# Kernel optimization log

Measured on AMD Instinct MI355X. Metric: run time of the kernel, lower is better.

## Reference

```python
import jax, jax.numpy as jnp
import numpy as np

D_MODEL = 1024
H = 16
D_K = D_MODEL // H
B = 2
S = 2048
NEG = -1e10


def setup_inputs() -> dict:
    key = jax.random.key(0)
    ks = jax.random.split(key, 12)
    sc = 1.0 / np.sqrt(D_MODEL)
    inp = {
        "q": jax.random.normal(ks[0], (B, S, D_MODEL), jnp.float32),
        "k": jax.random.normal(ks[1], (B, S, D_MODEL), jnp.float32),
        "v": jax.random.normal(ks[2], (B, S, D_MODEL), jnp.float32),
        # causal mask, broadcast over batch and heads
        "mask": jnp.tril(jnp.ones((S, S), jnp.int32))[None, None, :, :],
        "w_q": jax.random.normal(ks[3], (D_MODEL, D_MODEL), jnp.float32) * sc,
        "b_q": jax.random.normal(ks[4], (D_MODEL,), jnp.float32) * sc,
        "w_k": jax.random.normal(ks[5], (D_MODEL, D_MODEL), jnp.float32) * sc,
        "b_k": jax.random.normal(ks[6], (D_MODEL,), jnp.float32) * sc,
        "w_v": jax.random.normal(ks[7], (D_MODEL, D_MODEL), jnp.float32) * sc,
        "b_v": jax.random.normal(ks[8], (D_MODEL,), jnp.float32) * sc,
        "w_o": jax.random.normal(ks[9], (D_MODEL, D_MODEL), jnp.float32) * sc,
        "b_o": jax.random.normal(ks[10], (D_MODEL,), jnp.float32) * sc,
    }
    return inp


def _split_heads(x):
    # [B, S, D] -> [B, H, S, d_k]
    b, s, _ = x.shape
    return x.reshape(b, s, H, D_K).transpose(0, 2, 1, 3)


def reference(q, k, v, mask, w_q, b_q, w_k, b_k, w_v, b_v, w_o, b_o):
    # Linear projections (torch Linear: x @ W.T + b)
    qh = _split_heads(q @ w_q.T + b_q)
    kh = _split_heads(k @ w_k.T + b_k)
    vh = _split_heads(v @ w_v.T + b_v)
    scale = 1.0 / jnp.sqrt(jnp.asarray(D_K, qh.dtype))
    scores = jnp.einsum("bhqd,bhkd->bhqk", qh, kh) * scale
    scores = jnp.where(mask == 0, jnp.asarray(NEG, scores.dtype), scores)
    attn = jax.nn.softmax(scores, axis=-1)  # dropout=0.0 -> identity
    x = jnp.einsum("bhqk,bhkd->bhqd", attn, vh)
    x = x.transpose(0, 2, 1, 3).reshape(q.shape[0], -1, H * D_K)
    out = x @ w_o.T + b_o
    return (out, attn)
```

## Files before the change

kernel.cpp:

```cpp
#include <hip/hip_runtime.h>
#include <hip/hip_bf16.h>

typedef unsigned short u16;
typedef unsigned int u32;
typedef __attribute__((ext_vector_type(8))) short bf16x8;
typedef __attribute__((ext_vector_type(4))) float f32x4;

#define SEQ 2048
#define DM 1024
#define NH 16
#define DKK 64
#define NB 2

__device__ __forceinline__ u16 f2bf(float f) {
  union { float f; u32 u; } x; x.f = f;
  u32 r = x.u + 0x7FFFu + ((x.u >> 16) & 1u);
  return (u16)(r >> 16);
}

__device__ __forceinline__ void gl_lds16(const void* g, void* l) {
  __builtin_amdgcn_global_load_lds(
      (const __attribute__((address_space(1))) u32*)g,
      (__attribute__((address_space(3))) u32*)l, 16, 0, 0);
}

__device__ __forceinline__ void nt_store4(float* p, f32x4 v) {
  __builtin_nontemporal_store(v, (f32x4*)p);
}

#define MFMA16(a, b, c) __builtin_amdgcn_mfma_f32_16x16x32_bf16(a, b, c, 0, 0, 0)
#define VMCNT0() asm volatile("s_waitcnt vmcnt(0)" ::: "memory")
#define VMCNT4() asm volatile("s_waitcnt vmcnt(4)" ::: "memory")
#define SCHEDB() __builtin_amdgcn_sched_barrier(0)

struct CvtArgs {
  const float* in[7];
  u16* out[7];
  int n4[7];
};

__global__ __launch_bounds__(256) void cvt_all(CvtArgs a) {
  const int y = blockIdx.y;
  const float* in = a.in[y];
  u16* out = a.out[y];
  const int n4 = a.n4[y];
  int i = blockIdx.x * 256 + threadIdx.x;
  if (i >= n4) return;
  float4 v = ((const float4*)in)[i];
  ushort4 o;
  o.x = f2bf(v.x); o.y = f2bf(v.y); o.z = f2bf(v.z); o.w = f2bf(v.w);
  ((ushort4*)out)[i] = o;
}

struct ProjArgs {
  const u16* A;
  const u16* W;
  const float* bias;
  u16* Y;
  float scale;
};

__global__ __launch_bounds__(256) void proj_qkv(ProjArgs a0, ProjArgs a1,
                                                ProjArgs a2) {
  ProjArgs pa = (blockIdx.z == 0) ? a0 : (blockIdx.z == 1) ? a1 : a2;
  __shared__ __align__(16) u16 As[2][128 * 32];
  __shared__ __align__(16) u16 Bs[2][128 * 32];
  const int tid = threadIdx.x, lane = tid & 63, w = tid >> 6;
  const int lr = lane & 15, lg = lane >> 4;
  const int wr = w >> 1, wc = w & 1;
  const int c0 = blockIdx.x * 128, r0 = blockIdx.y * 128;
  f32x4 acc[4][4];
#pragma unroll
  for (int i = 0; i < 4; ++i)
#pragma unroll
    for (int j = 0; j < 4; ++j) acc[i][j] = (f32x4){0.f, 0.f, 0.f, 0.f};

  auto stage = [&](int k0, int buf) {
#pragma unroll
    for (int c = 0; c < 2; ++c) {
      int idx = tid + 256 * c;
      int row = idx >> 2, seg = idx & 3;
      gl_lds16(pa.A + (size_t)(r0 + row) * DM + k0 + seg * 8,
               (char*)As[buf] + idx * 16);
      gl_lds16(pa.W + (size_t)(c0 + row) * DM + k0 + seg * 8,
               (char*)Bs[buf] + idx * 16);
    }
  };

  stage(0, 0);
  __syncthreads();
  int buf = 0;
  const int NT = DM / 32;
  for (int t = 0; t < NT; ++t) {
    if (t + 1 < NT) stage((t + 1) * 32, buf ^ 1);
    bf16x8 a[4], b[4];
#pragma unroll
    for (int i = 0; i < 4; ++i) {
      int row = wr * 64 + i * 16 + lr;
      a[i] = *(const bf16x8*)((const char*)As[buf] + row * 64 + lg * 16);
    }
#pragma unroll
    for (int j = 0; j < 4; ++j) {
      int row = wc * 64 + j * 16 + lr;
      b[j] = *(const bf16x8*)((const char*)Bs[buf] + row * 64 + lg * 16);
    }
#pragma unroll
    for (int i = 0; i < 4; ++i)
#pragma unroll
      for (int j = 0; j < 4; ++j) acc[i][j] = MFMA16(a[i], b[j], acc[i][j]);
    __syncthreads();
    buf ^= 1;
  }
#pragma unroll
  for (int i = 0; i < 4; ++i)
#pragma unroll
    for (int j = 0; j < 4; ++j)
#pragma unroll
      for (int rg = 0; rg < 4; ++rg) {
        int row = r0 + wr * 64 + i * 16 + lg * 4 + rg;
        int col = c0 + wc * 64 + j * 16 + lr;
        float v = (acc[i][j][rg] + pa.bias[col]) * pa.scale;
        int bb = row >> 11, s = row & (SEQ - 1), h = col >> 6, d = col & 63;
        pa.Y[((size_t)(bb * NH + h) * SEQ + s) * DKK + d] = f2bf(v);
      }
}

__global__ __launch_bounds__(256) void mm_out(const u16* __restrict__ A,
                                              const u16* __restrict__ W,
                                              const float* __restrict__ bias,
                                              float* __restrict__ Y) {
  __shared__ __align__(16) u16 As[2][128 * 32];
  __shared__ __align__(16) u16 Bs[2][128 * 32];
  const int tid = threadIdx.x, lane = tid & 63, w = tid >> 6;
  const int lr = lane & 15, lg = lane >> 4;
  const int wr = w >> 1, wc = w & 1;
  const int c0 = blockIdx.x * 128, r0 = blockIdx.y * 128;
  f32x4 acc[4][4];
#pragma unroll
  for (int i = 0; i < 4; ++i)
#pragma unroll
    for (int j = 0; j < 4; ++j) acc[i][j] = (f32x4){0.f, 0.f, 0.f, 0.f};

  auto stage = [&](int k0, int buf) {
#pragma unroll
    for (int c = 0; c < 2; ++c) {
      int idx = tid + 256 * c;
      int row = idx >> 2, seg = idx & 3;
      gl_lds16(A + (size_t)(r0 + row) * DM + k0 + seg * 8,
               (char*)As[buf] + idx * 16);
      gl_lds16(W + (size_t)(c0 + row) * DM + k0 + seg * 8,
               (char*)Bs[buf] + idx * 16);
    }
  };

  stage(0, 0);
  __syncthreads();
  int buf = 0;
  const int NT = DM / 32;
  for (int t = 0; t < NT; ++t) {
    if (t + 1 < NT) stage((t + 1) * 32, buf ^ 1);
    bf16x8 a[4], b[4];
#pragma unroll
    for (int i = 0; i < 4; ++i) {
      int row = wr * 64 + i * 16 + lr;
      a[i] = *(const bf16x8*)((const char*)As[buf] + row * 64 + lg * 16);
    }
#pragma unroll
    for (int j = 0; j < 4; ++j) {
      int row = wc * 64 + j * 16 + lr;
      b[j] = *(const bf16x8*)((const char*)Bs[buf] + row * 64 + lg * 16);
    }
#pragma unroll
    for (int i = 0; i < 4; ++i)
#pragma unroll
      for (int j = 0; j < 4; ++j) acc[i][j] = MFMA16(a[i], b[j], acc[i][j]);
    __syncthreads();
    buf ^= 1;
  }
#pragma unroll
  for (int i = 0; i < 4; ++i)
#pragma unroll
    for (int j = 0; j < 4; ++j)
#pragma unroll
      for (int rg = 0; rg < 4; ++rg) {
        int row = r0 + wr * 64 + i * 16 + lg * 4 + rg;
        int col = c0 + wc * 64 + j * 16 + lr;
        Y[(size_t)row * DM + col] = acc[i][j][rg] + bias[col];
      }
}

__global__ __launch_bounds__(256) void transpose_v(const u16* __restrict__ Vh,
                                                   u16* __restrict__ Vt) {
  const int st = blockIdx.x, bh = blockIdx.y;
  const u16* src = Vh + ((size_t)bh * SEQ + st * 64) * DKK;
  u16* dst = Vt + (size_t)bh * DKK * SEQ + st * 64;
  __shared__ u16 T[64][68];
  const int tid = threadIdx.x;
#pragma unroll
  for (int c = 0; c < 4; ++c) {
    int idx = tid + 256 * c;
    int r = idx >> 4, seg = idx & 15;
    ushort4 v = *(const ushort4*)(src + r * 64 + seg * 4);
    *(ushort4*)&T[r][seg * 4] = v;
  }
  __syncthreads();
#pragma unroll
  for (int c = 0; c < 4; ++c) {
    int idx = tid + 256 * c;
    int d = idx >> 4, sseg = idx & 15;
    ushort4 o;
    o.x = T[sseg * 4 + 0][d]; o.y = T[sseg * 4 + 1][d];
    o.z = T[sseg * 4 + 2][d]; o.w = T[sseg * 4 + 3][d];
    *(ushort4*)(dst + (size_t)d * SEQ + sseg * 4) = o;
  }
}

__global__ __launch_bounds__(256) void flash_attn(const u16* __restrict__ Qh,
                                                  const u16* __restrict__ Kh,
                                                  const u16* __restrict__ Vt,
                                                  u16* __restrict__ X,
                                                  float* __restrict__ attn) {
  const int lin = (int)(blockIdx.y * gridDim.x + blockIdx.x);
  const int swz = (lin & 7) * 128 + (lin >> 3);
  const int qi = 31 - (swz & 31);
  const int bh = swz >> 5;
  const int q0 = qi * 64;
  const u16* Qb = Qh + (size_t)bh * SEQ * DKK;
  const u16* Kb = Kh + (size_t)bh * SEQ * DKK;
  const u16* Vb = Vt + (size_t)bh * DKK * SEQ;
  float* attb = attn + (size_t)bh * SEQ * SEQ;
  const int tid = threadIdx.x, lane = tid & 63, w = tid >> 6;
  const int lr = lane & 15, lg = lane >> 4;

  __shared__ __align__(16) u16 Ks[2][64 * 64];
  __shared__ __align__(16) u16 Vs[2][64 * 64];
  __shared__ __align__(16) u16 Ps[4 * 16 * 64];

  bf16x8 frQ[2];
#pragma unroll
  for (int kc = 0; kc < 2; ++kc) {
    int r = q0 + w * 16 + lr;
    frQ[kc] = *(const bf16x8*)(Qb + (size_t)r * DKK + kc * 32 + lg * 8);
  }

  const int qglob = q0 + w * 16 + lr;
  const int wmax = q0 + w * 16 + 15;
  const int nkv = qi + 1;

  auto stageK = [&](int j, int buf) {
    const int kv0 = j * 64;
#pragma unroll
    for (int c = 0; c < 2; ++c) {
      int idx = tid + 256 * c;
      int row = idx >> 3, sq = idx & 7;
      int seg = sq ^ (row & 7);
      gl_lds16(Kb + (size_t)(kv0 + row) * DKK + seg * 8,
               (char*)Ks[buf] + idx * 16);
    }
  };
  auto stageV = [&](int j, int buf) {
    const int kv0 = j * 64;
#pragma unroll
    for (int c = 0; c < 2; ++c) {
      int idx = tid + 256 * c;
      int row = idx >> 3, sq = idx & 7;
      int seg = sq ^ (row & 7);
      gl_lds16(Vb + (size_t)row * SEQ + kv0 + seg * 8,
               (char*)Vs[buf] + idx * 16);
    }
  };

  float rs = 0.f;
  stageK(0, 0);
  VMCNT0();
  __builtin_amdgcn_s_barrier();
  SCHEDB();
  for (int j = 0; j < nkv; ++j) {
    const int buf = j & 1;
    const int kv0 = j * 64;
    if (j + 1 < nkv) stageK(j + 1, buf ^ 1);
    if (kv0 <= wmax) {
      __builtin_amdgcn_s_setprio(1);
#pragma unroll
      for (int ci = 0; ci < 4; ++ci) {
        bf16x8 aK[2];
#pragma unroll
        for (int kc = 0; kc < 2; ++kc) {
          int row = ci * 16 + lr;
          int q = (kc * 4 + lg) ^ (row & 7);
          aK[kc] = *(const bf16x8*)((const char*)Ks[buf] + row * 128 + q * 16);
        }
        f32x4 a = (f32x4){0.f, 0.f, 0.f, 0.f};
        a = MFMA16(aK[0], frQ[0], a);
        a = MFMA16(aK[1], frQ[1], a);
#pragma unroll
        for (int rg = 0; rg < 4; ++rg) {
          int kvglob = kv0 + ci * 16 + lg * 4 + rg;
          rs += (kvglob <= qglob) ? __expf(a[rg]) : 0.f;
        }
      }
      __builtin_amdgcn_s_setprio(0);
    }
    VMCNT0();
    __builtin_amdgcn_s_barrier();
    SCHEDB();
  }
  rs += __shfl_xor(rs, 16);
  rs += __shfl_xor(rs, 32);
  const float vinv = 1.f / rs;

  f32x4 accO[4];
#pragma unroll
  for (int ci = 0; ci < 4; ++ci) accO[ci] = (f32x4){0.f, 0.f, 0.f, 0.f};

  stageK(0, 0);
  stageV(0, 0);
  VMCNT0();
  __builtin_amdgcn_s_barrier();
  SCHEDB();
  for (int j = 0; j < nkv; ++j) {
    const int buf = j & 1;
    const int kv0 = j * 64;
    if (j + 1 < nkv) {
      stageK(j + 1, buf ^ 1);
      stageV(j + 1, buf ^ 1);
    }
    if (kv0 <= wmax) {
      __builtin_amdgcn_s_setprio(1);
      f32x4 sf[4];
#pragma unroll
      for (int ci = 0; ci < 4; ++ci) {
        bf16x8 aK[2];
#pragma unroll
        for (int kc = 0; kc < 2; ++kc) {
          int row = ci * 16 + lr;
          int q = (kc * 4 + lg) ^ (row & 7);
          aK[kc] = *(const bf16x8*)((const char*)Ks[buf] + row * 128 + q * 16);
        }
        f32x4 a = (f32x4){0.f, 0.f, 0.f, 0.f};
        a = MFMA16(aK[0], frQ[0], a);
        a = MFMA16(aK[1], frQ[1], a);
        sf[ci] = a;
      }
      float* orow = attb + (size_t)qglob * SEQ;
#pragma unroll
      for (int ci = 0; ci < 4; ++ci) {
        float p[4];
#pragma unroll
        for (int rg = 0; rg < 4; ++rg) {
          int kvglob = kv0 + ci * 16 + lg * 4 + rg;
          p[rg] = (kvglob <= qglob) ? __expf(sf[ci][rg]) * vinv : 0.f;
        }
        f32x4 o = {p[0], p[1], p[2], p[3]};
        nt_store4(orow + kv0 + ci * 16 + lg * 4, o);
        u32 lo = (u32)f2bf(p[0]) | ((u32)f2bf(p[1]) << 16);
        u32 hi = (u32)f2bf(p[2]) | ((u32)f2bf(p[3]) << 16);
        int c16 = (ci * 2 + (lg >> 1)) ^ (lr & 7);
        char* dst = (char*)Ps + w * 2048 + lr * 128 + c16 * 16 + (lg & 1) * 8;
        *(uint2*)dst = (uint2){lo, hi};
      }
#pragma unroll
      for (int kvc = 0; kvc < 2; ++kvc) {
        int c16a = (kvc * 4 + lg) ^ (lr & 7);
        bf16x8 aP =
            *(const bf16x8*)((const char*)Ps + w * 2048 + lr * 128 + c16a * 16);
#pragma unroll
        for (int ci = 0; ci < 4; ++ci) {
          int row = ci * 16 + lr;
          int q2 = (kvc * 4 + lg) ^ (row & 7);
          bf16x8 bV =
              *(const bf16x8*)((const char*)Vs[buf] + row * 128 + q2 * 16);
          accO[ci] = MFMA16(aP, bV, accO[ci]);
        }
      }
      __builtin_amdgcn_s_setprio(0);
    } else {
      const f32x4 z = {0.f, 0.f, 0.f, 0.f};
      float* orow = attb + (size_t)qglob * SEQ;
#pragma unroll
      for (int ci = 0; ci < 4; ++ci)
        nt_store4(orow + kv0 + ci * 16 + lg * 4, z);
    }
    VMCNT4();
    __builtin_amdgcn_s_barrier();
    SCHEDB();
  }

  {
    const f32x4 z = {0.f, 0.f, 0.f, 0.f};
    float* orow = attb + (size_t)qglob * SEQ;
    for (int j = nkv; j < SEQ / 64; ++j) {
      const int kv0 = j * 64;
#pragma unroll
      for (int ci = 0; ci < 4; ++ci)
        nt_store4(orow + kv0 + ci * 16 + lg * 4, z);
    }
  }

  const int b = bh >> 4, h = bh & (NH - 1);
#pragma unroll
  for (int ci = 0; ci < 4; ++ci)
#pragma unroll
    for (int rg = 0; rg < 4; ++rg) {
      int srow = q0 + w * 16 + lg * 4 + rg;
      int col = h * DKK + ci * 16 + lr;
      X[((size_t)(b * SEQ + srow)) * DM + col] = f2bf(accO[ci][rg]);
    }
}

extern "C" void kernel_launch(void* const* d_in, const int* in_sizes, int n_in,
                              void* d_out, int out_size, void* d_ws,
                              size_t ws_size, hipStream_t stream) {
  const float* q = (const float*)d_in[0];
  const float* k = (const float*)d_in[1];
  const float* v = (const float*)d_in[2];
  const float* w_q = (const float*)d_in[4];
  const float* b_q = (const float*)d_in[5];
  const float* w_k = (const float*)d_in[6];
  const float* b_k = (const float*)d_in[7];
  const float* w_v = (const float*)d_in[8];
  const float* b_v = (const float*)d_in[9];
  const float* w_o = (const float*)d_in[10];
  const float* b_o = (const float*)d_in[11];

  float* out = (float*)d_out;
  float* attn = out + (size_t)NB * SEQ * DM;

  const size_t MB = 1u << 20;
  char* ws = (char*)d_ws;
  u16* qb = (u16*)(ws);
  u16* kb = (u16*)(ws + 8 * MB);
  u16* vb = (u16*)(ws + 16 * MB);
  u16* Qh = (u16*)(ws + 24 * MB);
  u16* Kh = (u16*)(ws + 32 * MB);
  u16* Vh = (u16*)(ws + 40 * MB);
  u16* wqb = (u16*)(ws + 48 * MB);
  u16* wkb = (u16*)(ws + 50 * MB);
  u16* wvb = (u16*)(ws + 52 * MB);
  u16* wob = (u16*)(ws + 54 * MB);
  u16* Vt = qb;
  u16* X = vb;

  dim3 blk(256);
  const int n4_qkv = NB * SEQ * DM / 4;
  const int n4_w = DM * DM / 4;

  CvtArgs ca;
  ca.in[0] = q;   ca.out[0] = qb;  ca.n4[0] = n4_qkv;
  ca.in[1] = k;   ca.out[1] = kb;  ca.n4[1] = n4_qkv;
  ca.in[2] = v;   ca.out[2] = vb;  ca.n4[2] = n4_qkv;
  ca.in[3] = w_q; ca.out[3] = wqb; ca.n4[3] = n4_w;
  ca.in[4] = w_k; ca.out[4] = wkb; ca.n4[4] = n4_w;
  ca.in[5] = w_v; ca.out[5] = wvb; ca.n4[5] = n4_w;
  ca.in[6] = w_o; ca.out[6] = wob; ca.n4[6] = n4_w;
  cvt_all<<<dim3((n4_qkv + 255) / 256, 7), blk, 0, stream>>>(ca);

  ProjArgs aq = {qb, wqb, b_q, Qh, 0.125f};
  ProjArgs ak = {kb, wkb, b_k, Kh, 1.0f};
  ProjArgs av = {vb, wvb, b_v, Vh, 1.0f};
  proj_qkv<<<dim3(DM / 128, NB * SEQ / 128, 3), blk, 0, stream>>>(aq, ak, av);

  transpose_v<<<dim3(SEQ / 64, NB * NH), blk, 0, stream>>>(Vh, Vt);

  flash_attn<<<dim3(SEQ / 64, NB * NH), blk, 0, stream>>>(Qh, Kh, Vt, X, attn);

  mm_out<<<dim3(DM / 128, NB * SEQ / 128), blk, 0, stream>>>(X, wob, b_o, out);
}
```

Baseline: 325.9 us.

## Fuse all stages into one persistent megakernel with grid-wide atomic barriers

After: 736.6 us. 126% more time.

```diff
diff --git a/kernel.cpp b/kernel.cpp
--- a/kernel.cpp
+++ b/kernel.cpp
@@ -11,6 +11,7 @@
 #define NH 16
 #define DKK 64
 #define NB 2
+#define NBLK 512
 
 __device__ __forceinline__ u16 f2bf(float f) {
   union { float f; u32 u; } x; x.f = f;
@@ -24,120 +25,47 @@
       (__attribute__((address_space(3))) u32*)l, 16, 0, 0);
 }
 
-__device__ __forceinline__ void nt_store4(float* p, f32x4 v) {
-  __builtin_nontemporal_store(v, (f32x4*)p);
-}
-
 #define MFMA16(a, b, c) __builtin_amdgcn_mfma_f32_16x16x32_bf16(a, b, c, 0, 0, 0)
 #define VMCNT0() asm volatile("s_waitcnt vmcnt(0)" ::: "memory")
-#define VMCNT4() asm volatile("s_waitcnt vmcnt(4)" ::: "memory")
 #define SCHEDB() __builtin_amdgcn_sched_barrier(0)
 
-struct CvtArgs {
-  const float* in[7];
-  u16* out[7];
-  int n4[7];
+__device__ __forceinline__ void gbar(int* cnt, int idx) {
+  __syncthreads();
+  if (threadIdx.x == 0) {
+    __threadfence();
+    __hip_atomic_fetch_add(&cnt[idx], 1, __ATOMIC_RELEASE,
+                           __HIP_MEMORY_SCOPE_AGENT);
+    while (__hip_atomic_load(&cnt[idx], __ATOMIC_ACQUIRE,
+                             __HIP_MEMORY_SCOPE_AGENT) < NBLK) {
+      __builtin_amdgcn_s_sleep(8);
+    }
+    __threadfence();
+  }
+  __syncthreads();
+}
+
+struct MegaArgs {
+  const float *q, *k, *v;
+  const float *wq, *bq, *wk, *bk, *wv, *bv, *wo, *bo;
+  u16 *qb, *kb, *vb;
+  u16 *Qh, *Kh, *Vh;
+  u16 *wqb, *wkb, *wvb, *wob;
+  u16 *Vt, *X;
+  float *out, *attn;
+  int *cnt;
 };
 
-__global__ __launch_bounds__(256) void cvt_all(CvtArgs a) {
-  const int y = blockIdx.y;
-  const float* in = a.in[y];
-  u16* out = a.out[y];
-  const int n4 = a.n4[y];
-  int i = blockIdx.x * 256 + threadIdx.x;
-  if (i >= n4) return;
-  float4 v = ((const float4*)in)[i];
-  ushort4 o;
-  o.x = f2bf(v.x); o.y = f2bf(v.y); o.z = f2bf(v.z); o.w = f2bf(v.w);
-  ((ushort4*)out)[i] = o;
-}
-
-struct ProjArgs {
-  const u16* A;
-  const u16* W;
-  const float* bias;
-  u16* Y;
-  float scale;
-};
-
-__global__ __launch_bounds__(256) void proj_qkv(ProjArgs a0, ProjArgs a1,
-                                                ProjArgs a2) {
-  ProjArgs pa = (blockIdx.z == 0) ? a0 : (blockIdx.z == 1) ? a1 : a2;
-  __shared__ __align__(16) u16 As[2][128 * 32];
-  __shared__ __align__(16) u16 Bs[2][128 * 32];
-  const int tid = threadIdx.x, lane = tid & 63, w = tid >> 6;
+template <int MODE>
+__device__ void gemm128x64(const u16* __restrict__ A, const u16* __restrict__ Wm,
+                           const float* __restrict__ bias, u16* Yh, float* Yf,
+                           float scale, int r0, int c0, char* LDSp, int tid) {
+  char* As = LDSp;
+  char* Bs = LDSp + 16384;
+  const int lane = tid & 63, w = tid >> 6;
   const int lr = lane & 15, lg = lane >> 4;
-  const int wr = w >> 1, wc = w & 1;
-  const int c0 = blockIdx.x * 128, r0 = blockIdx.y * 128;
-  f32x4 acc[4][4];
-#pragma unroll
-  for (int i = 0; i < 4; ++i)
-#pragma unroll
-    for (int j = 0; j < 4; ++j) acc[i][j] = (f32x4){0.f, 0.f, 0.f, 0.f};
-
-  auto stage = [&](int k0, int buf) {
-#pragma unroll
-    for (int c = 0; c < 2; ++c) {
-      int idx = tid + 256 * c;
-      int row = idx >> 2, seg = idx & 3;
-      gl_lds16(pa.A + (size_t)(r0 + row) * DM + k0 + seg * 8,
-               (char*)As[buf] + idx * 16);
-      gl_lds16(pa.W + (size_t)(c0 + row) * DM + k0 + seg * 8,
-               (char*)Bs[buf] + idx * 16);
-    }
-  };
-
-  stage(0, 0);
-  __syncthreads();
-  int buf = 0;
-  const int NT = DM / 32;
-  for (int t = 0; t < NT; ++t) {
-    if (t + 1 < NT) stage((t + 1) * 32, buf ^ 1);
-    bf16x8 a[4], b[4];
-#pragma unroll
-    for (int i = 0; i < 4; ++i) {
-      int row = wr * 64 + i * 16 + lr;
-      a[i] = *(const bf16x8*)((const char*)As[buf] + row * 64 + lg * 16);
-    }
-#pragma unroll
-    for (int j = 0; j < 4; ++j) {
-      int row = wc * 64 + j * 16 + lr;
-      b[j] = *(const bf16x8*)((const char*)Bs[buf] + row * 64 + lg * 16);
-    }
-#pragma unroll
-    for (int i = 0; i < 4; ++i)
-#pragma unroll
-      for (int j = 0; j < 4; ++j) acc[i][j] = MFMA16(a[i], b[j], acc[i][j]);
-    __syncthreads();
-    buf ^= 1;
-  }
-#pragma unroll
-  for (int i = 0; i < 4; ++i)
-#pragma unroll
-    for (int j = 0; j < 4; ++j)
-#pragma unroll
-      for (int rg = 0; rg < 4; ++rg) {
-        int row = r0 + wr * 64 + i * 16 + lg * 4 + rg;
-        int col = c0 + wc * 64 + j * 16 + lr;
-        float v = (acc[i][j][rg] + pa.bias[col]) * pa.scale;
-        int bb = row >> 11, s = row & (SEQ - 1), h = col >> 6, d = col & 63;
-        pa.Y[((size_t)(bb * NH + h) * SEQ + s) * DKK + d] = f2bf(v);
-      }
-}
-
-__global__ __launch_bounds__(256) void mm_out(const u16* __restrict__ A,
-                                              const u16* __restrict__ W,
-                                              const float* __restrict__ bias,
-                                              float* __restrict__ Y) {
-  __shared__ __align__(16) u16 As[2][128 * 32];
-  __shared__ __align__(16) u16 Bs[2][128 * 32];
-  const int tid = threadIdx.x, lane = tid & 63, w = tid >> 6;
-  const int lr = lane & 15, lg = lane >> 4;
-  const int wr = w >> 1, wc = w & 1;
-  const int c0 = blockIdx.x * 128, r0 = blockIdx.y * 128;
-  f32x4 acc[4][4];
-#pragma unroll
-  for (int i = 0; i < 4; ++i)
+  f32x4 acc[2][4];
+#pragma unroll
+  for (int i = 0; i < 2; ++i)
 #pragma unroll
     for (int j = 0; j < 4; ++j) acc[i][j] = (f32x4){0.f, 0.f, 0.f, 0.f};
 
@@ -147,105 +75,76 @@
       int idx = tid + 256 * c;
       int row = idx >> 2, seg = idx & 3;
       gl_lds16(A + (size_t)(r0 + row) * DM + k0 + seg * 8,
-               (char*)As[buf] + idx * 16);
-      gl_lds16(W + (size_t)(c0 + row) * DM + k0 + seg * 8,
-               (char*)Bs[buf] + idx * 16);
+               As + buf * 8192 + idx * 16);
+    }
+    {
+      int row = tid >> 2, seg = tid & 3;
+      gl_lds16(Wm + (size_t)(c0 + row) * DM + k0 + seg * 8,
+               Bs + buf * 4096 + tid * 16);
     }
   };
 
   stage(0, 0);
   __syncthreads();
   int buf = 0;
-  const int NT = DM / 32;
-  for (int t = 0; t < NT; ++t) {
-    if (t + 1 < NT) stage((t + 1) * 32, buf ^ 1);
-    bf16x8 a[4], b[4];
-#pragma unroll
-    for (int i = 0; i < 4; ++i) {
-      int row = wr * 64 + i * 16 + lr;
-      a[i] = *(const bf16x8*)((const char*)As[buf] + row * 64 + lg * 16);
+#pragma unroll 1
+  for (int t = 0; t < DM / 32; ++t) {
+    if (t + 1 < DM / 32) stage((t + 1) * 32, buf ^ 1);
+    bf16x8 aa[2], bb[4];
+#pragma unroll
+    for (int i = 0; i < 2; ++i) {
+      int row = w * 32 + i * 16 + lr;
+      aa[i] = *(const bf16x8*)(As + buf * 8192 + row * 64 + lg * 16);
     }
 #pragma unroll
     for (int j = 0; j < 4; ++j) {
-      int row = wc * 64 + j * 16 + lr;
-      b[j] = *(const bf16x8*)((const char*)Bs[buf] + row * 64 + lg * 16);
-    }
-#pragma unroll
-    for (int i = 0; i < 4; ++i)
-#pragma unroll
-      for (int j = 0; j < 4; ++j) acc[i][j] = MFMA16(a[i], b[j], acc[i][j]);
+      int row2 = j * 16 + lr;
+      bb[j] = *(const bf16x8*)(Bs + buf * 4096 + row2 * 64 + lg * 16);
+    }
+#pragma unroll
+    for (int i = 0; i < 2; ++i)
+#pragma unroll
+      for (int j = 0; j < 4; ++j) acc[i][j] = MFMA16(aa[i], bb[j], acc[i][j]);
     __syncthreads();
     buf ^= 1;
   }
 #pragma unroll
-  for (int i = 0; i < 4; ++i)
+  for (int i = 0; i < 2; ++i)
 #pragma unroll
     for (int j = 0; j < 4; ++j)
 #pragma unroll
       for (int rg = 0; rg < 4; ++rg) {
-        int row = r0 + wr * 64 + i * 16 + lg * 4 + rg;
-        int col = c0 + wc * 64 + j * 16 + lr;
-        Y[(size_t)row * DM + col] = acc[i][j][rg] + bias[col];
-      }
-}
-
-__global__ __launch_bounds__(256) void transpose_v(const u16* __restrict__ Vh,
-                                                   u16* __restrict__ Vt) {
-  const int st = blockIdx.x, bh = blockIdx.y;
-  const u16* src = Vh + ((size_t)bh * SEQ + st * 64) * DKK;
-  u16* dst = Vt + (size_t)bh * DKK * SEQ + st * 64;
-  __shared__ u16 T[64][68];
-  const int tid = threadIdx.x;
-#pragma unroll
-  for (int c = 0; c < 4; ++c) {
-    int idx = tid + 256 * c;
-    int r = idx >> 4, seg = idx & 15;
-    ushort4 v = *(const ushort4*)(src + r * 64 + seg * 4);
-    *(ushort4*)&T[r][seg * 4] = v;
-  }
-  __syncthreads();
-#pragma unroll
-  for (int c = 0; c < 4; ++c) {
-    int idx = tid + 256 * c;
-    int d = idx >> 4, sseg = idx & 15;
-    ushort4 o;
-    o.x = T[sseg * 4 + 0][d]; o.y = T[sseg * 4 + 1][d];
-    o.z = T[sseg * 4 + 2][d]; o.w = T[sseg * 4 + 3][d];
-    *(ushort4*)(dst + (size_t)d * SEQ + sseg * 4) = o;
-  }
-}
-
-__global__ __launch_bounds__(256) void flash_attn(const u16* __restrict__ Qh,
-                                                  const u16* __restrict__ Kh,
-                                                  const u16* __restrict__ Vt,
-                                                  u16* __restrict__ X,
-                                                  float* __restrict__ attn) {
-  const int lin = (int)(blockIdx.y * gridDim.x + blockIdx.x);
-  const int swz = (lin & 7) * 128 + (lin >> 3);
-  const int qi = 31 - (swz & 31);
-  const int bh = swz >> 5;
+        int row = r0 + w * 32 + i * 16 + lg * 4 + rg;
+        int col = c0 + j * 16 + lr;
+        if (MODE == 0) {
+          float v = (acc[i][j][rg] + bias[col]) * scale;
+          int bb2 = row >> 11, s = row & (SEQ - 1);
+          int h = col >> 6, d = col & 63;
+          Yh[((size_t)(bb2 * NH + h) * SEQ + s) * DKK + d] = f2bf(v);
+        } else {
+          Yf[(size_t)row * DM + col] = acc[i][j][rg] + bias[col];
+        }
+      }
+}
+
+__device__ void flash64(const u16* __restrict__ Qb, const u16* __restrict__ Kb,
+                        const u16* __restrict__ Vb, u16* __restrict__ X,
+                        float* __restrict__ attb, int bh, int qi, char* LDSp,
+                        int tid) {
+  char* Ks = LDSp;
+  char* Vs = LDSp + 16384;
+  char* Ps = LDSp + 32768;
+  const int lane = tid & 63, w = tid >> 6;
+  const int lr = lane & 15, lg = lane >> 4;
   const int q0 = qi * 64;
-  const u16* Qb = Qh + (size_t)bh * SEQ * DKK;
-  const u16* Kb = Kh + (size_t)bh * SEQ * DKK;
-  const u16* Vb = Vt + (size_t)bh * DKK * SEQ;
-  float* attb = attn + (size_t)bh * SEQ * SEQ;
-  const int tid = threadIdx.x, lane = tid & 63, w = tid >> 6;
-  const int lr = lane & 15, lg = lane >> 4;
-
-  __shared__ __align__(16) u16 Ks[2][64 * 64];
-  __shared__ __align__(16) u16 Vs[2][64 * 64];
-  __shared__ __align__(16) u16 Ps[4 * 16 * 64];
-
-  bf16x8 frQ[2];
-#pragma unroll
-  for (int kc = 0; kc < 2; ++kc) {
-    int r = q0 + w * 16 + lr;
-    frQ[kc] = *(const bf16x8*)(Qb + (size_t)r * DKK + kc * 32 + lg * 8);
-  }
-
   const int qglob = q0 + w * 16 + lr;
   const int wmax = q0 + w * 16 + 15;
   const int nkv = qi + 1;
+
+  bf16x8 frQ[2];
+#pragma unroll
+  for (int kc = 0; kc < 2; ++kc)
+    frQ[kc] = *(const bf16x8*)(Qb + (size_t)qglob * DKK + kc * 32 + lg * 8);
 
   auto stageK = [&](int j, int buf) {
     const int kv0 = j * 64;
@@ -255,7 +154,7 @@
       int row = idx >> 3, sq = idx & 7;
       int seg = sq ^ (row & 7);
       gl_lds16(Kb + (size_t)(kv0 + row) * DKK + seg * 8,
-               (char*)Ks[buf] + idx * 16);
+               Ks + buf * 8192 + idx * 16);
     }
   };
   auto stageV = [&](int j, int buf) {
@@ -266,7 +165,7 @@
       int row = idx >> 3, sq = idx & 7;
       int seg = sq ^ (row & 7);
       gl_lds16(Vb + (size_t)row * SEQ + kv0 + seg * 8,
-               (char*)Vs[buf] + idx * 16);
+               Vs + buf * 8192 + idx * 16);
     }
   };
 
@@ -287,8 +186,8 @@
 #pragma unroll
         for (int kc = 0; kc < 2; ++kc) {
           int row = ci * 16 + lr;
-          int q = (kc * 4 + lg) ^ (row & 7);
-          aK[kc] = *(const bf16x8*)((const char*)Ks[buf] + row * 128 + q * 16);
+          int qq = (kc * 4 + lg) ^ (row & 7);
+          aK[kc] = *(const bf16x8*)(Ks + buf * 8192 + row * 128 + qq * 16);
         }
         f32x4 a = (f32x4){0.f, 0.f, 0.f, 0.f};
         a = MFMA16(aK[0], frQ[0], a);
@@ -325,6 +224,7 @@
       stageK(j + 1, buf ^ 1);
       stageV(j + 1, buf ^ 1);
     }
+    float* orow = attb + (size_t)qglob * SEQ;
     if (kv0 <= wmax) {
       __builtin_amdgcn_s_setprio(1);
       f32x4 sf[4];
@@ -334,15 +234,14 @@
 #pragma unroll
         for (int kc = 0; kc < 2; ++kc) {
           int row = ci * 16 + lr;
-          int q = (kc * 4 + lg) ^ (row & 7);
-          aK[kc] = *(const bf16x8*)((const char*)Ks[buf] + row * 128 + q * 16);
+          int qq = (kc * 4 + lg) ^ (row & 7);
+          aK[kc] = *(const bf16x8*)(Ks + buf * 8192 + row * 128 + qq * 16);
         }
         f32x4 a = (f32x4){0.f, 0.f, 0.f, 0.f};
         a = MFMA16(aK[0], frQ[0], a);
         a = MFMA16(aK[1], frQ[1], a);
         sf[ci] = a;
       }
-      float* orow = attb + (size_t)qglob * SEQ;
 #pragma unroll
       for (int ci = 0; ci < 4; ++ci) {
         float p[4];
@@ -352,36 +251,33 @@
           p[rg] = (kvglob <= qglob) ? __expf(sf[ci][rg]) * vinv : 0.f;
         }
         f32x4 o = {p[0], p[1], p[2], p[3]};
-        nt_store4(orow + kv0 + ci * 16 + lg * 4, o);
+        *(f32x4*)(orow + kv0 + ci * 16 + lg * 4) = o;
         u32 lo = (u32)f2bf(p[0]) | ((u32)f2bf(p[1]) << 16);
         u32 hi = (u32)f2bf(p[2]) | ((u32)f2bf(p[3]) << 16);
         int c16 = (ci * 2 + (lg >> 1)) ^ (lr & 7);
-        char* dst = (char*)Ps + w * 2048 + lr * 128 + c16 * 16 + (lg & 1) * 8;
+        char* dst = Ps + w * 2048 + lr * 128 + c16 * 16 + (lg & 1) * 8;
         *(uint2*)dst = (uint2){lo, hi};
       }
 #pragma unroll
       for (int kvc = 0; kvc < 2; ++kvc) {
         int c16a = (kvc * 4 + lg) ^ (lr & 7);
-        bf16x8 aP =
-            *(const bf16x8*)((const char*)Ps + w * 2048 + lr * 128 + c16a * 16);
+        bf16x8 aP = *(const bf16x8*)(Ps + w * 2048 + lr * 128 + c16a * 16);
 #pragma unroll
         for (int ci = 0; ci < 4; ++ci) {
           int row = ci * 16 + lr;
           int q2 = (kvc * 4 + lg) ^ (row & 7);
-          bf16x8 bV =
-              *(const bf16x8*)((const char*)Vs[buf] + row * 128 + q2 * 16);
+          bf16x8 bV = *(const bf16x8*)(Vs + buf * 8192 + row * 128 + q2 * 16);
           accO[ci] = MFMA16(aP, bV, accO[ci]);
         }
       }
       __builtin_amdgcn_s_setprio(0);
     } else {
       const f32x4 z = {0.f, 0.f, 0.f, 0.f};
-      float* orow = attb + (size_t)qglob * SEQ;
 #pragma unroll
       for (int ci = 0; ci < 4; ++ci)
-        nt_store4(orow + kv0 + ci * 16 + lg * 4, z);
-    }
-    VMCNT4();
+        *(f32x4*)(orow + kv0 + ci * 16 + lg * 4) = z;
+    }
+    VMCNT0();
     __builtin_amdgcn_s_barrier();
     SCHEDB();
   }
@@ -393,7 +289,7 @@
       const int kv0 = j * 64;
 #pragma unroll
       for (int ci = 0; ci < 4; ++ci)
-        nt_store4(orow + kv0 + ci * 16 + lg * 4, z);
+        *(f32x4*)(orow + kv0 + ci * 16 + lg * 4) = z;
     }
   }
 
@@ -408,61 +304,139 @@
     }
 }
 
+__global__ __launch_bounds__(256, 2) void mega(MegaArgs a) {
+  __shared__ __align__(16) char LDS[40 * 1024];
+  const int tid = threadIdx.x, bid = (int)blockIdx.x;
+
+  {
+    const int base = bid * 256 + tid;
+#pragma unroll 4
+    for (int it = 0; it < 32; ++it) {
+      int i = base + it * (NBLK * 256);
+      const float* in;
+      u16* outp;
+      int loc;
+      if (i < 3145728) {
+        int t = i >> 20;
+        loc = i & 1048575;
+        in = (t == 0) ? a.q : (t == 1) ? a.k : a.v;
+        outp = (t == 0) ? a.qb : (t == 1) ? a.kb : a.vb;
+      } else {
+        int j2 = i - 3145728;
+        int t = j2 >> 18;
+        loc = j2 & 262143;
+        in = (t == 0) ? a.wq : (t == 1) ? a.wk : (t == 2) ? a.wv : a.wo;
+        outp = (t == 0) ? a.wqb : (t == 1) ? a.wkb : (t == 2) ? a.wvb : a.wob;
+      }
+      float4 vv = ((const float4*)in)[loc];
+      ushort4 o;
+      o.x = f2bf(vv.x); o.y = f2bf(vv.y); o.z = f2bf(vv.z); o.w = f2bf(vv.w);
+      ((ushort4*)outp)[loc] = o;
+    }
+  }
+  gbar(a.cnt, 0);
+
+  for (int s = 0; s < 3; ++s) {
+    int job = bid + s * NBLK;
+    int g = job >> 9;
+    int jl = job & 511;
+    int ct = jl & 15, rt = jl >> 4;
+    const u16* A = (g == 0) ? a.qb : (g == 1) ? a.kb : a.vb;
+    const u16* Wm = (g == 0) ? a.wqb : (g == 1) ? a.wkb : a.wvb;
+    const float* bias = (g == 0) ? a.bq : (g == 1) ? a.bk : a.bv;
+    u16* Y = (g == 0) ? a.Qh : (g == 1) ? a.Kh : a.Vh;
+    float scale = (g == 0) ? 0.125f : 1.0f;
+    gemm128x64<0>(A, Wm, bias, Y, nullptr, scale, rt * 128, ct * 64, LDS, tid);
+    __syncthreads();
+  }
+  gbar(a.cnt, 1);
+
+  for (int s = 0; s < 2; ++s) {
+    int job = bid + s * NBLK;
+    int st = job & 31, bh = job >> 5;
+    const u16* src = a.Vh + ((size_t)bh * SEQ + st * 64) * DKK;
+    u16* dst = a.Vt + (size_t)bh * DKK * SEQ + st * 64;
+    u16(*T)[68] = (u16(*)[68])LDS;
+#pragma unroll
+    for (int c = 0; c < 4; ++c) {
+      int idx = tid + 256 * c;
+      int r = idx >> 4, seg = idx & 15;
+      ushort4 v = *(const ushort4*)(src + r * 64 + seg * 4);
+      *(ushort4*)&T[r][seg * 4] = v;
+    }
+    __syncthreads();
+#pragma unroll
+    for (int c = 0; c < 4; ++c) {
+      int idx = tid + 256 * c;
+      int d = idx >> 4, sseg = idx & 15;
+      ushort4 o;
+      o.x = T[sseg * 4 + 0][d]; o.y = T[sseg * 4 + 1][d];
+      o.z = T[sseg * 4 + 2][d]; o.w = T[sseg * 4 + 3][d];
+      *(ushort4*)(dst + (size_t)d * SEQ + sseg * 4) = o;
+    }
+    __syncthreads();
+  }
+  gbar(a.cnt, 2);
+
+  {
+    const int iq = bid & 15, bh = bid >> 4;
+    const u16* Qb = a.Qh + (size_t)bh * SEQ * DKK;
+    const u16* Kb = a.Kh + (size_t)bh * SEQ * DKK;
+    const u16* Vb = a.Vt + (size_t)bh * DKK * SEQ;
+    float* attb = a.attn + (size_t)bh * SEQ * SEQ;
+#pragma unroll 1
+    for (int pp = 0; pp < 2; ++pp) {
+      int qi = pp ? (31 - iq) : iq;
+      flash64(Qb, Kb, Vb, a.X, attb, bh, qi, LDS, tid);
+      __syncthreads();
+    }
+  }
+  gbar(a.cnt, 3);
+
+  {
+    int ct = bid & 15, rt = bid >> 4;
+    gemm128x64<1>(a.X, a.wob, a.bo, nullptr, a.out, 1.0f, rt * 128, ct * 64,
+                  LDS, tid);
+  }
+}
+
 extern "C" void kernel_launch(void* const* d_in, const int* in_sizes, int n_in,
                               void* d_out, int out_size, void* d_ws,
                               size_t ws_size, hipStream_t stream) {
-  const float* q = (const float*)d_in[0];
-  const float* k = (const float*)d_in[1];
-  const float* v = (const float*)d_in[2];
-  const float* w_q = (const float*)d_in[4];
-  const float* b_q = (const float*)d_in[5];
-  const float* w_k = (const float*)d_in[6];
-  const float* b_k = (const float*)d_in[7];
-  const float* w_v = (const float*)d_in[8];
-  const float* b_v = (const float*)d_in[9];
-  const float* w_o = (const float*)d_in[10];
-  const float* b_o = (const float*)d_in[11];
+  MegaArgs ma;
+  ma.q = (const float*)d_in[0];
+  ma.k = (const float*)d_in[1];
+  ma.v = (const float*)d_in[2];
+  ma.wq = (const float*)d_in[4];
+  ma.bq = (const float*)d_in[5];
+  ma.wk = (const float*)d_in[6];
+  ma.bk = (const float*)d_in[7];
+  ma.wv = (const float*)d_in[8];
+  ma.bv = (const float*)d_in[9];
+  ma.wo = (const float*)d_in[10];
+  ma.bo = (const float*)d_in[11];
 
   float* out = (float*)d_out;
-  float* attn = out + (size_t)NB * SEQ * DM;
+  ma.out = out;
+  ma.attn = out + (size_t)NB * SEQ * DM;
 
   const size_t MB = 1u << 20;
   char* ws = (char*)d_ws;
-  u16* qb = (u16*)(ws);
-  u16* kb = (u16*)(ws + 8 * MB);
-  u16* vb = (u16*)(ws + 16 * MB);
-  u16* Qh = (u16*)(ws + 24 * MB);
-  u16* Kh = (u16*)(ws + 32 * MB);
-  u16* Vh = (u16*)(ws + 40 * MB);
-  u16* wqb = (u16*)(ws + 48 * MB);
-  u16* wkb = (u16*)(ws + 50 * MB);
-  u16* wvb = (u16*)(ws + 52 * MB);
-  u16* wob = (u16*)(ws + 54 * MB);
-  u16* Vt = qb;
-  u16* X = vb;
-
-  dim3 blk(256);
-  const int n4_qkv = NB * SEQ * DM / 4;
-  const int n4_w = DM * DM / 4;
-
-  CvtArgs ca;
-  ca.in[0] = q;   ca.out[0] = qb;  ca.n4[0] = n4_qkv;
-  ca.in[1] = k;   ca.out[1] = kb;  ca.n4[1] = n4_qkv;
-  ca.in[2] = v;   ca.out[2] = vb;  ca.n4[2] = n4_qkv;
-  ca.in[3] = w_q; ca.out[3] = wqb; ca.n4[3] = n4_w;
-  ca.in[4] = w_k; ca.out[4] = wkb; ca.n4[4] = n4_w;
-  ca.in[5] = w_v; ca.out[5] = wvb; ca.n4[5] = n4_w;
-  ca.in[6] = w_o; ca.out[6] = wob; ca.n4[6] = n4_w;
-  cvt_all<<<dim3((n4_qkv + 255) / 256, 7), blk, 0, stream>>>(ca);
-
-  ProjArgs aq = {qb, wqb, b_q, Qh, 0.125f};
-  ProjArgs ak = {kb, wkb, b_k, Kh, 1.0f};
-  ProjArgs av = {vb, wvb, b_v, Vh, 1.0f};
-  proj_qkv<<<dim3(DM / 128, NB * SEQ / 128, 3), blk, 0, stream>>>(aq, ak, av);
-
-  transpose_v<<<dim3(SEQ / 64, NB * NH), blk, 0, stream>>>(Vh, Vt);
-
-  flash_attn<<<dim3(SEQ / 64, NB * NH), blk, 0, stream>>>(Qh, Kh, Vt, X, attn);
-
-  mm_out<<<dim3(DM / 128, NB * SEQ / 128), blk, 0, stream>>>(X, wob, b_o, out);
-}
+  ma.qb = (u16*)(ws);
+  ma.kb = (u16*)(ws + 8 * MB);
+  ma.vb = (u16*)(ws + 16 * MB);
+  ma.Qh = (u16*)(ws + 24 * MB);
+  ma.Kh = (u16*)(ws + 32 * MB);
+  ma.Vh = (u16*)(ws + 40 * MB);
+  ma.wqb = (u16*)(ws + 48 * MB);
+  ma.wkb = (u16*)(ws + 50 * MB);
+  ma.wvb = (u16*)(ws + 52 * MB);
+  ma.wob = (u16*)(ws + 54 * MB);
+  ma.Vt = ma.qb;
+  ma.X = ma.vb;
+  ma.cnt = (int*)(ws + 56 * MB);
+
+  hipMemsetAsync(ma.cnt, 0, 64, stream);
+
+  mega<<<dim3(NBLK), dim3(256), 0, stream>>>(ma);
+}
```
